# Kernel tuning notes

Hardware: AMD Instinct MI355X
Metric: run time of the kernel (lower is better)

The kernel has to match this reference:

```python
import jax, jax.numpy as jnp
import numpy as np

UNITS = 2048

def _cat_complex(Wr, Wi):
    # real-matrix representation of complex matmul: [[Wr, -Wi], [Wi, Wr]]
    top = jnp.concatenate([Wr, -Wi], axis=-1)
    bot = jnp.concatenate([Wi, Wr], axis=-1)
    return jnp.concatenate([top, bot], axis=0)

def _hard_sigmoid(x):
    return jnp.clip(0.2 * x + 0.5, 0.0, 1.0)

def setup_inputs() -> dict:
    key = jax.random.key(0)
    ks = jax.random.split(key, 8)
    B, IN2, U3 = 1024, 4096, 3 * UNITS
    s_in = 1.0 / np.sqrt(IN2)
    s_h = 1.0 / np.sqrt(2 * UNITS)
    return {
        "inputs": jax.random.normal(ks[0], (B, IN2), jnp.float32),
        "h_tm1": jax.random.normal(ks[1], (B, 2 * UNITS), jnp.float32),
        "real_kernel": jax.random.normal(ks[2], (IN2 // 2, U3), jnp.float32) * s_in,
        "imaginary_kernel": jax.random.normal(ks[3], (IN2 // 2, U3), jnp.float32) * s_in,
        "real_recurrent_kernel": jax.random.normal(ks[4], (UNITS, U3), jnp.float32) * s_h,
        "imaginary_recurrent_kernel": jax.random.normal(ks[5], (UNITS, U3), jnp.float32) * s_h,
        "real_bias": jax.random.normal(ks[6], (U3,), jnp.float32) * 0.01,
        "imaginary_bias": jax.random.normal(ks[7], (U3,), jnp.float32) * 0.01,
    }

def reference(inputs, h_tm1, real_kernel, imaginary_kernel,
              real_recurrent_kernel, imaginary_recurrent_kernel,
              real_bias, imaginary_bias):
    u = UNITS
    # per-gate complex kernels in real [[Wr,-Wi],[Wi,Wr]] form
    Kz = _cat_complex(real_kernel[:, :u], imaginary_kernel[:, :u])
    Kr = _cat_complex(real_kernel[:, u:2 * u], imaginary_kernel[:, u:2 * u])
    Kh = _cat_complex(real_kernel[:, 2 * u:], imaginary_kernel[:, 2 * u:])
    Rz = _cat_complex(real_recurrent_kernel[:, :u], imaginary_recurrent_kernel[:, :u])
    Rr = _cat_complex(real_recurrent_kernel[:, u:2 * u], imaginary_recurrent_kernel[:, u:2 * u])
    Rh = _cat_complex(real_recurrent_kernel[:, 2 * u:], imaginary_recurrent_kernel[:, 2 * u:])
    bz = jnp.concatenate([real_bias[:u], imaginary_bias[:u]])
    br = jnp.concatenate([real_bias[u:2 * u], imaginary_bias[u:2 * u]])
    bh = jnp.concatenate([real_bias[2 * u:], imaginary_bias[2 * u:]])
    # implementation=1, reset_after=False, no dropout
    x_z = inputs @ Kz + bz
    x_r = inputs @ Kr + br
    x_h = inputs @ Kh + bh
    z = _hard_sigmoid(x_z + h_tm1 @ Rz)
    r = _hard_sigmoid(x_r + h_tm1 @ Rr)
    hh = jnp.tanh(x_h + (r * h_tm1) @ Rh)
    h = z * h_tm1 + (1.0 - z) * hh
    return h
```

## Files before the change

### kernel.cpp

```cpp
#include <hip/hip_runtime.h>

typedef _Float16 half8  __attribute__((ext_vector_type(8)));
typedef _Float16 half4v __attribute__((ext_vector_type(4)));
typedef _Float16 half2v __attribute__((ext_vector_type(2)));
typedef float    float4v __attribute__((ext_vector_type(4)));

__device__ __forceinline__ float hsig(float x) {
  return fminf(fmaxf(fmaf(x, 0.2f, 0.5f), 0.0f), 1.0f);
}

__global__ __launch_bounds__(256) void cvt_pair(const float* __restrict__ src,
                                                _Float16* __restrict__ d1,
                                                _Float16* __restrict__ d2) {
  int i = blockIdx.x * blockDim.x + threadIdx.x;
  int base = i * 4;
  int j = base & 4095;
  float s = (j < 2048) ? -1.0f : 1.0f;
  float4 v = *(const float4*)&src[base];
  half4v h1 = {(_Float16)v.x, (_Float16)v.y, (_Float16)v.z, (_Float16)v.w};
  half4v h2 = {(_Float16)(s * v.x), (_Float16)(s * v.y), (_Float16)(s * v.z), (_Float16)(s * v.w)};
  *(half4v*)&d1[base] = h1;
  *(half4v*)&d2[base] = h2;
}

__global__ __launch_bounds__(256) void transpose_cast(
    const float* __restrict__ s0, const float* __restrict__ s1,
    const float* __restrict__ s2, const float* __restrict__ s3,
    _Float16* __restrict__ d0, _Float16* __restrict__ d1m,
    _Float16* __restrict__ d2m, _Float16* __restrict__ d3m)
{
  __shared__ float tile[64][65];
  const float* srcs[4] = {s0, s1, s2, s3};
  _Float16*    dsts[4] = {d0, d1m, d2m, d3m};
  const float* src = srcs[blockIdx.z];
  _Float16*    dst = dsts[blockIdx.z];

  const int tid = threadIdx.x;
  const int k0 = blockIdx.x * 64;
  const int j0 = blockIdx.y * 64;

  const int tx = tid & 63, ty = tid >> 6;
#pragma unroll
  for (int r = 0; r < 64; r += 4)
    tile[r + ty][tx] = src[(size_t)(k0 + r + ty) * 6144 + j0 + tx];
  __syncthreads();

  const int txk = (tid & 31) * 2;
  const int tyn = tid >> 5;
#pragma unroll
  for (int r = 0; r < 64; r += 8) {
    int jl = r + tyn;
    half2v p = {(_Float16)tile[txk][jl], (_Float16)tile[txk + 1][jl]};
    *(half2v*)&dst[(size_t)(j0 + jl) * 2048 + k0 + txk] = p;
  }
}

__global__ __launch_bounds__(256) void rgate(const _Float16* __restrict__ xacc,
                                             const float* __restrict__ h,
                                             _Float16* __restrict__ A1r,
                                             _Float16* __restrict__ A2r) {
  int i = blockIdx.x * blockDim.x + threadIdx.x;
  int base = i * 4;
  int m = base >> 12;
  int j = base & 4095;
  float s = (j < 2048) ? -1.0f : 1.0f;
  half4v rp = *(const half4v*)&xacc[(size_t)m * 12288 + 4096 + j];
  float4 hv = *(const float4*)&h[base];
  float p0 = hsig((float)rp[0]) * hv.x;
  float p1 = hsig((float)rp[1]) * hv.y;
  float p2 = hsig((float)rp[2]) * hv.z;
  float p3 = hsig((float)rp[3]) * hv.w;
  half4v o1 = {(_Float16)p0, (_Float16)p1, (_Float16)p2, (_Float16)p3};
  half4v o2 = {(_Float16)(s * p0), (_Float16)(s * p1), (_Float16)(s * p2), (_Float16)(s * p3)};
  *(half4v*)&A1r[base] = o1;
  *(half4v*)&A2r[base] = o2;
}

__global__ __launch_bounds__(256) void combine(const _Float16* __restrict__ xacc,
                                               const _Float16* __restrict__ P0,
                                               const _Float16* __restrict__ P1,
                                               const float* __restrict__ h,
                                               float* __restrict__ out) {
  int i = blockIdx.x * blockDim.x + threadIdx.x;
  int base = i * 4;
  int m = base >> 12;
  int j = base & 4095;
  half4v zv = *(const half4v*)&xacc[(size_t)m * 12288 + j];
  half4v xh = *(const half4v*)&xacc[(size_t)m * 12288 + 8192 + j];
  half4v p0 = *(const half4v*)&P0[base];
  half4v p1 = *(const half4v*)&P1[base];
  float4 hv = *(const float4*)&h[base];
  float4 o;
  {
    float z = hsig((float)zv[0]); float t = tanhf((float)xh[0] + (float)p0[0] + (float)p1[0]);
    o.x = z * hv.x + (1.0f - z) * t;
  }
  {
    float z = hsig((float)zv[1]); float t = tanhf((float)xh[1] + (float)p0[1] + (float)p1[1]);
    o.y = z * hv.y + (1.0f - z) * t;
  }
  {
    float z = hsig((float)zv[2]); float t = tanhf((float)xh[2] + (float)p0[2] + (float)p1[2]);
    o.z = z * hv.z + (1.0f - z) * t;
  }
  {
    float z = hsig((float)zv[3]); float t = tanhf((float)xh[3] + (float)p0[3] + (float)p1[3]);
    o.w = z * hv.w + (1.0f - z) * t;
  }
  *(float4*)&out[base] = o;
}

template<int FINAL>
__global__ __launch_bounds__(256, 3) void gemm_big(
    const _Float16* __restrict__ Ax1, const _Float16* __restrict__ Ax2,
    const _Float16* __restrict__ Ah1, const _Float16* __restrict__ Ah2,
    const _Float16* __restrict__ WKr, const _Float16* __restrict__ WKi,
    const _Float16* __restrict__ WRr, const _Float16* __restrict__ WRi,
    _Float16* __restrict__ xacc,
    _Float16* __restrict__ P0, _Float16* __restrict__ P1,
    const float* __restrict__ rbias, const float* __restrict__ ibias)
{
  __shared__ __align__(16) _Float16 lds[16384];
  const int tid  = threadIdx.x;
  const int lane = tid & 63;
  const int wave = tid >> 6;
  const int quad = lane >> 4;
  const int r16  = lane & 15;
  const int wm = (wave >> 1) * 64;
  const int wn = (wave & 1) * 64;
  const int mbase = blockIdx.y * 128;
  const int nbase = blockIdx.x * 128;

  const int  gate   = nbase >> 12;
  const bool hi     = (nbase & 2048) != 0;
  const int  jprime = nbase & 2047;

  int nph;
  const _Float16* pA[4];
  const _Float16* pB[4];
  if (FINAL) {
    nph = 1;
    const _Float16* Ax = hi ? Ax2 : Ax1;
    const _Float16* BL = hi ? WKi : WKr;
    const _Float16* BH = hi ? WKr : WKi;
    if (blockIdx.z == 0) {
      pA[0] = Ax + (size_t)mbase * 4096;
      pB[0] = BL + (size_t)jprime * 2048;
    } else {
      pA[0] = Ax + (size_t)mbase * 4096 + 2048;
      pB[0] = BH + (size_t)jprime * 2048;
    }
  } else {
    const size_t browK = (size_t)(gate * 2048 + jprime) * 2048;
    const _Float16* Ax = hi ? Ax2 : Ax1;
    const _Float16* KL = hi ? WKi : WKr;
    const _Float16* KH = hi ? WKr : WKi;
    pA[0] = Ax + (size_t)mbase * 4096;      pB[0] = KL + browK;
    pA[1] = pA[0] + 2048;                   pB[1] = KH + browK;
    if (gate < 2) {
      nph = 4;
      const _Float16* Ah = hi ? Ah2 : Ah1;
      const _Float16* RL = hi ? WRi : WRr;
      const _Float16* RH = hi ? WRr : WRi;
      pA[2] = Ah + (size_t)mbase * 4096;    pB[2] = RL + browK;
      pA[3] = pA[2] + 2048;                 pB[3] = RH + browK;
    } else {
      nph = 2;
    }
  }

  float4v acc[4][4];
#pragma unroll
  for (int i = 0; i < 4; ++i)
#pragma unroll
    for (int j = 0; j < 4; ++j) acc[i][j] = (float4v){0.f, 0.f, 0.f, 0.f};

  int offA[4], offB[4], ldsA[4], ldsB[4];
#pragma unroll
  for (int i = 0; i < 4; ++i) {
    int c = i * 256 + tid;
    int row = c >> 3;
    int sw = (c & 7) ^ (row & 7);
    offA[i] = row * 4096 + sw * 8;
    offB[i] = row * 2048 + sw * 8;
    ldsA[i] = c * 8;
    ldsB[i] = 8192 + c * 8;
  }

#pragma unroll 1
  for (int p = 0; p < 4; ++p) {
    if (p >= nph) break;
    const _Float16* Ab = pA[p];
    const _Float16* Bb = pB[p];
#pragma unroll 1
    for (int it = 0; it < 32; ++it) {
#pragma unroll
      for (int i = 0; i < 4; ++i)
        __builtin_amdgcn_global_load_lds(
            (__attribute__((address_space(1))) void*)(Ab + offA[i]),
            (__attribute__((address_space(3))) void*)&lds[ldsA[i]], 16, 0, 0);
#pragma unroll
      for (int i = 0; i < 4; ++i)
        __builtin_amdgcn_global_load_lds(
            (__attribute__((address_space(1))) void*)(Bb + offB[i]),
            (__attribute__((address_space(3))) void*)&lds[ldsB[i]], 16, 0, 0);
      Ab += 64;
      Bb += 64;
      __syncthreads();
#pragma unroll
      for (int ks = 0; ks < 2; ++ks) {
        half8 af[4], bf[4];
        int akg = ks * 4 + quad;
#pragma unroll
        for (int t = 0; t < 4; ++t) {
          int arow = wm + t * 16 + r16;
          af[t] = *(const half8*)&lds[(arow * 8 + (akg ^ (arow & 7))) * 8];
          int brow = wn + t * 16 + r16;
          bf[t] = *(const half8*)&lds[8192 + (brow * 8 + (akg ^ (brow & 7))) * 8];
        }
#pragma unroll
        for (int mt = 0; mt < 4; ++mt)
#pragma unroll
          for (int nt = 0; nt < 4; ++nt)
            acc[mt][nt] = __builtin_amdgcn_mfma_f32_16x16x32_f16(af[mt], bf[nt], acc[mt][nt], 0, 0, 0);
      }
      __syncthreads();
    }
  }

  const int mrow0 = mbase + wm + quad * 4;
  const int ncol0 = nbase + wn + r16;
  if (!FINAL) {
#pragma unroll
    for (int nt = 0; nt < 4; ++nt) {
      int n = ncol0 + nt * 16;
      int g = n >> 12, j = n & 4095;
      float b = (j < 2048) ? rbias[g * 2048 + j] : ibias[g * 2048 + j - 2048];
#pragma unroll
      for (int mt = 0; mt < 4; ++mt)
#pragma unroll
        for (int e = 0; e < 4; ++e) {
          int m = mrow0 + mt * 16 + e;
          xacc[(size_t)m * 12288 + n] = (_Float16)(acc[mt][nt][e] + b);
        }
    }
  } else {
    _Float16* P = blockIdx.z ? P1 : P0;
#pragma unroll
    for (int nt = 0; nt < 4; ++nt) {
      int n = ncol0 + nt * 16;
#pragma unroll
      for (int mt = 0; mt < 4; ++mt)
#pragma unroll
        for (int e = 0; e < 4; ++e) {
          int m = mrow0 + mt * 16 + e;
          P[(size_t)m * 4096 + n] = (_Float16)acc[mt][nt][e];
        }
    }
  }
}

extern "C" void kernel_launch(void* const* d_in, const int* in_sizes, int n_in,
                              void* d_out, int out_size, void* d_ws, size_t ws_size,
                              hipStream_t stream) {
  const float* inputs = (const float*)d_in[0];
  const float* h_tm1  = (const float*)d_in[1];
  const float* rk     = (const float*)d_in[2];
  const float* ik     = (const float*)d_in[3];
  const float* rrk    = (const float*)d_in[4];
  const float* irk    = (const float*)d_in[5];
  const float* rb     = (const float*)d_in[6];
  const float* ib     = (const float*)d_in[7];
  float* out = (float*)d_out;

  char* ws = (char*)d_ws;
  _Float16* WrK  = (_Float16*)(ws + 0);
  _Float16* WiK  = (_Float16*)(ws + 25165824);
  _Float16* WrR  = (_Float16*)(ws + 50331648);
  _Float16* WiR  = (_Float16*)(ws + 75497472);
  _Float16* A1x  = (_Float16*)(ws + 100663296);
  _Float16* A2x  = (_Float16*)(ws + 109051904);
  _Float16* A1h  = (_Float16*)(ws + 117440512);
  _Float16* A2h  = (_Float16*)(ws + 125829120);
  _Float16* xacc = (_Float16*)(ws + 134217728);
  _Float16* A1r  = A1x;
  _Float16* A2r  = A2x;
  _Float16* P0   = A1h;
  _Float16* P1   = A2h;

  cvt_pair<<<4096, 256, 0, stream>>>(inputs, A1x, A2x);
  cvt_pair<<<4096, 256, 0, stream>>>(h_tm1, A1h, A2h);
  transpose_cast<<<dim3(32, 96, 4), 256, 0, stream>>>(rk, ik, rrk, irk, WrK, WiK, WrR, WiR);
  gemm_big<0><<<dim3(96, 8), 256, 0, stream>>>(A1x, A2x, A1h, A2h, WrK, WiK, WrR, WiR,
                                               xacc, nullptr, nullptr, rb, ib);
  rgate<<<4096, 256, 0, stream>>>(xacc, h_tm1, A1r, A2r);
  gemm_big<1><<<dim3(32, 8, 2), 256, 0, stream>>>(A1r, A2r, nullptr, nullptr,
                                                  WrR + (size_t)4096 * 2048,
                                                  WiR + (size_t)4096 * 2048,
                                                  nullptr, nullptr, nullptr, P0, P1,
                                                  nullptr, nullptr);
  combine<<<4096, 256, 0, stream>>>(xacc, P0, P1, h_tm1, out);
}
```

Baseline: 504.5 us.

## Fuse final GRU combine into candidate GEMM epilogue and merge conversion launches

Replaces the split-K final GEMM (two fp16 partial outputs plus a separate combine kernel) with a single GEMM over both K halves using 64x128 tiles, whose epilogue applies the hard sigmoid, tanh and gated blend and writes the output directly. It also merges the two input conversion launches into one 2D launch and widens transpose_cast stores to 8 halves per thread. This removes the partial-sum round trip through global memory and two kernel launches. The trade-off is that the final GEMM now has a longer K loop per block with no split-K parallelism, and its epilogue does strided scalar loads from xacc and h_tm1.

```diff
diff --git a/kernel.cpp b/kernel.cpp
--- a/kernel.cpp
+++ b/kernel.cpp
@@ -9,9 +9,13 @@
   return fminf(fmaxf(fmaf(x, 0.2f, 0.5f), 0.0f), 1.0f);
 }
 
-__global__ __launch_bounds__(256) void cvt_pair(const float* __restrict__ src,
-                                                _Float16* __restrict__ d1,
-                                                _Float16* __restrict__ d2) {
+__global__ __launch_bounds__(256) void cvt_pair2(
+    const float* __restrict__ s0, const float* __restrict__ s1,
+    _Float16* __restrict__ d1a, _Float16* __restrict__ d2a,
+    _Float16* __restrict__ d1b, _Float16* __restrict__ d2b) {
+  const float* src = blockIdx.y ? s1 : s0;
+  _Float16* d1 = blockIdx.y ? d1b : d1a;
+  _Float16* d2 = blockIdx.y ? d2b : d2a;
   int i = blockIdx.x * blockDim.x + threadIdx.x;
   int base = i * 4;
   int j = base & 4095;
@@ -45,13 +49,15 @@
     tile[r + ty][tx] = src[(size_t)(k0 + r + ty) * 6144 + j0 + tx];
   __syncthreads();
 
-  const int txk = (tid & 31) * 2;
-  const int tyn = tid >> 5;
-#pragma unroll
-  for (int r = 0; r < 64; r += 8) {
-    int jl = r + tyn;
-    half2v p = {(_Float16)tile[txk][jl], (_Float16)tile[txk + 1][jl]};
-    *(half2v*)&dst[(size_t)(j0 + jl) * 2048 + k0 + txk] = p;
+  const int kc = tid & 7;
+  const int jr = tid >> 3;
+#pragma unroll
+  for (int r = 0; r < 64; r += 32) {
+    int jl = r + jr;
+    half8 p;
+#pragma unroll
+    for (int i = 0; i < 8; ++i) p[i] = (_Float16)tile[kc * 8 + i][jl];
+    *(half8*)&dst[(size_t)(j0 + jl) * 2048 + k0 + kc * 8] = p;
   }
 }
 
@@ -76,48 +82,12 @@
   *(half4v*)&A2r[base] = o2;
 }
 
-__global__ __launch_bounds__(256) void combine(const _Float16* __restrict__ xacc,
-                                               const _Float16* __restrict__ P0,
-                                               const _Float16* __restrict__ P1,
-                                               const float* __restrict__ h,
-                                               float* __restrict__ out) {
-  int i = blockIdx.x * blockDim.x + threadIdx.x;
-  int base = i * 4;
-  int m = base >> 12;
-  int j = base & 4095;
-  half4v zv = *(const half4v*)&xacc[(size_t)m * 12288 + j];
-  half4v xh = *(const half4v*)&xacc[(size_t)m * 12288 + 8192 + j];
-  half4v p0 = *(const half4v*)&P0[base];
-  half4v p1 = *(const half4v*)&P1[base];
-  float4 hv = *(const float4*)&h[base];
-  float4 o;
-  {
-    float z = hsig((float)zv[0]); float t = tanhf((float)xh[0] + (float)p0[0] + (float)p1[0]);
-    o.x = z * hv.x + (1.0f - z) * t;
-  }
-  {
-    float z = hsig((float)zv[1]); float t = tanhf((float)xh[1] + (float)p0[1] + (float)p1[1]);
-    o.y = z * hv.y + (1.0f - z) * t;
-  }
-  {
-    float z = hsig((float)zv[2]); float t = tanhf((float)xh[2] + (float)p0[2] + (float)p1[2]);
-    o.z = z * hv.z + (1.0f - z) * t;
-  }
-  {
-    float z = hsig((float)zv[3]); float t = tanhf((float)xh[3] + (float)p0[3] + (float)p1[3]);
-    o.w = z * hv.w + (1.0f - z) * t;
-  }
-  *(float4*)&out[base] = o;
-}
-
-template<int FINAL>
-__global__ __launch_bounds__(256, 3) void gemm_big(
+__global__ __launch_bounds__(256, 3) void gemm_fused(
     const _Float16* __restrict__ Ax1, const _Float16* __restrict__ Ax2,
     const _Float16* __restrict__ Ah1, const _Float16* __restrict__ Ah2,
     const _Float16* __restrict__ WKr, const _Float16* __restrict__ WKi,
     const _Float16* __restrict__ WRr, const _Float16* __restrict__ WRi,
     _Float16* __restrict__ xacc,
-    _Float16* __restrict__ P0, _Float16* __restrict__ P1,
     const float* __restrict__ rbias, const float* __restrict__ ibias)
 {
   __shared__ __align__(16) _Float16 lds[16384];
@@ -134,24 +104,12 @@
   const int  gate   = nbase >> 12;
   const bool hi     = (nbase & 2048) != 0;
   const int  jprime = nbase & 2047;
+  const size_t browK = (size_t)(gate * 2048 + jprime) * 2048;
 
   int nph;
   const _Float16* pA[4];
   const _Float16* pB[4];
-  if (FINAL) {
-    nph = 1;
-    const _Float16* Ax = hi ? Ax2 : Ax1;
-    const _Float16* BL = hi ? WKi : WKr;
-    const _Float16* BH = hi ? WKr : WKi;
-    if (blockIdx.z == 0) {
-      pA[0] = Ax + (size_t)mbase * 4096;
-      pB[0] = BL + (size_t)jprime * 2048;
-    } else {
-      pA[0] = Ax + (size_t)mbase * 4096 + 2048;
-      pB[0] = BH + (size_t)jprime * 2048;
-    }
-  } else {
-    const size_t browK = (size_t)(gate * 2048 + jprime) * 2048;
+  {
     const _Float16* Ax = hi ? Ax2 : Ax1;
     const _Float16* KL = hi ? WKi : WKr;
     const _Float16* KH = hi ? WKr : WKi;
@@ -230,33 +188,132 @@
 
   const int mrow0 = mbase + wm + quad * 4;
   const int ncol0 = nbase + wn + r16;
-  if (!FINAL) {
-#pragma unroll
-    for (int nt = 0; nt < 4; ++nt) {
-      int n = ncol0 + nt * 16;
-      int g = n >> 12, j = n & 4095;
-      float b = (j < 2048) ? rbias[g * 2048 + j] : ibias[g * 2048 + j - 2048];
-#pragma unroll
-      for (int mt = 0; mt < 4; ++mt)
-#pragma unroll
-        for (int e = 0; e < 4; ++e) {
-          int m = mrow0 + mt * 16 + e;
-          xacc[(size_t)m * 12288 + n] = (_Float16)(acc[mt][nt][e] + b);
+#pragma unroll
+  for (int nt = 0; nt < 4; ++nt) {
+    int n = ncol0 + nt * 16;
+    int g = n >> 12, j = n & 4095;
+    float b = (j < 2048) ? rbias[g * 2048 + j] : ibias[g * 2048 + j - 2048];
+#pragma unroll
+    for (int mt = 0; mt < 4; ++mt)
+#pragma unroll
+      for (int e = 0; e < 4; ++e) {
+        int m = mrow0 + mt * 16 + e;
+        xacc[(size_t)m * 12288 + n] = (_Float16)(acc[mt][nt][e] + b);
+      }
+  }
+}
+
+__global__ __launch_bounds__(256, 4) void gemm_final(
+    const _Float16* __restrict__ A1, const _Float16* __restrict__ A2,
+    const _Float16* __restrict__ Wr, const _Float16* __restrict__ Wi,
+    const _Float16* __restrict__ xacc, const float* __restrict__ h_tm1,
+    float* __restrict__ out)
+{
+  __shared__ __align__(16) _Float16 lds[12288];
+  const int tid  = threadIdx.x;
+  const int lane = tid & 63;
+  const int wave = tid >> 6;
+  const int quad = lane >> 4;
+  const int r16  = lane & 15;
+  const int wm = (wave >> 1) * 32;
+  const int wn = (wave & 1) * 64;
+  const int mbase = blockIdx.y * 64;
+  const int nbase = blockIdx.x * 128;
+
+  const bool hi     = (nbase & 2048) != 0;
+  const int  jprime = nbase & 2047;
+  const _Float16* A  = hi ? A2 : A1;
+  const _Float16* BL = hi ? Wi : Wr;
+  const _Float16* BH = hi ? Wr : Wi;
+
+  const _Float16* pA[2] = { A + (size_t)mbase * 4096,
+                            A + (size_t)mbase * 4096 + 2048 };
+  const _Float16* pB[2] = { BL + (size_t)jprime * 2048,
+                            BH + (size_t)jprime * 2048 };
+
+  float4v acc[2][4];
+#pragma unroll
+  for (int i = 0; i < 2; ++i)
+#pragma unroll
+    for (int j = 0; j < 4; ++j) acc[i][j] = (float4v){0.f, 0.f, 0.f, 0.f};
+
+  int offA[2], ldsA[2], offB[4], ldsB[4];
+#pragma unroll
+  for (int i = 0; i < 2; ++i) {
+    int c = i * 256 + tid;
+    int row = c >> 3;
+    int sw = (c & 7) ^ (row & 7);
+    offA[i] = row * 4096 + sw * 8;
+    ldsA[i] = c * 8;
+  }
+#pragma unroll
+  for (int i = 0; i < 4; ++i) {
+    int c = i * 256 + tid;
+    int row = c >> 3;
+    int sw = (c & 7) ^ (row & 7);
+    offB[i] = row * 2048 + sw * 8;
+    ldsB[i] = 4096 + c * 8;
+  }
+
+#pragma unroll 1
+  for (int p = 0; p < 2; ++p) {
+    const _Float16* Ab = pA[p];
+    const _Float16* Bb = pB[p];
+#pragma unroll 1
+    for (int it = 0; it < 32; ++it) {
+#pragma unroll
+      for (int i = 0; i < 2; ++i)
+        __builtin_amdgcn_global_load_lds(
+            (__attribute__((address_space(1))) void*)(Ab + offA[i]),
+            (__attribute__((address_space(3))) void*)&lds[ldsA[i]], 16, 0, 0);
+#pragma unroll
+      for (int i = 0; i < 4; ++i)
+        __builtin_amdgcn_global_load_lds(
+            (__attribute__((address_space(1))) void*)(Bb + offB[i]),
+            (__attribute__((address_space(3))) void*)&lds[ldsB[i]], 16, 0, 0);
+      Ab += 64;
+      Bb += 64;
+      __syncthreads();
+#pragma unroll
+      for (int ks = 0; ks < 2; ++ks) {
+        half8 af[2], bf[4];
+        int akg = ks * 4 + quad;
+#pragma unroll
+        for (int t = 0; t < 2; ++t) {
+          int arow = wm + t * 16 + r16;
+          af[t] = *(const half8*)&lds[(arow * 8 + (akg ^ (arow & 7))) * 8];
         }
+#pragma unroll
+        for (int t = 0; t < 4; ++t) {
+          int brow = wn + t * 16 + r16;
+          bf[t] = *(const half8*)&lds[4096 + (brow * 8 + (akg ^ (brow & 7))) * 8];
+        }
+#pragma unroll
+        for (int mt = 0; mt < 2; ++mt)
+#pragma unroll
+          for (int nt = 0; nt < 4; ++nt)
+            acc[mt][nt] = __builtin_amdgcn_mfma_f32_16x16x32_f16(af[mt], bf[nt], acc[mt][nt], 0, 0, 0);
+      }
+      __syncthreads();
     }
-  } else {
-    _Float16* P = blockIdx.z ? P1 : P0;
-#pragma unroll
-    for (int nt = 0; nt < 4; ++nt) {
-      int n = ncol0 + nt * 16;
-#pragma unroll
-      for (int mt = 0; mt < 4; ++mt)
-#pragma unroll
-        for (int e = 0; e < 4; ++e) {
-          int m = mrow0 + mt * 16 + e;
-          P[(size_t)m * 4096 + n] = (_Float16)acc[mt][nt][e];
-        }
-    }
+  }
+
+  const int mrow0 = mbase + wm + quad * 4;
+  const int ncol0 = nbase + wn + r16;
+#pragma unroll
+  for (int nt = 0; nt < 4; ++nt) {
+    int n = ncol0 + nt * 16;
+#pragma unroll
+    for (int mt = 0; mt < 2; ++mt)
+#pragma unroll
+      for (int e = 0; e < 4; ++e) {
+        int m = mrow0 + mt * 16 + e;
+        float z  = hsig((float)xacc[(size_t)m * 12288 + n]);
+        float xh = (float)xacc[(size_t)m * 12288 + 8192 + n];
+        float hh = tanhf(xh + acc[mt][nt][e]);
+        float ht = h_tm1[(size_t)m * 4096 + n];
+        out[(size_t)m * 4096 + n] = z * ht + (1.0f - z) * hh;
+      }
   }
 }
 
@@ -285,19 +342,14 @@
   _Float16* xacc = (_Float16*)(ws + 134217728);
   _Float16* A1r  = A1x;
   _Float16* A2r  = A2x;
-  _Float16* P0   = A1h;
-  _Float16* P1   = A2h;
-
-  cvt_pair<<<4096, 256, 0, stream>>>(inputs, A1x, A2x);
-  cvt_pair<<<4096, 256, 0, stream>>>(h_tm1, A1h, A2h);
+
+  cvt_pair2<<<dim3(4096, 2), 256, 0, stream>>>(inputs, h_tm1, A1x, A2x, A1h, A2h);
   transpose_cast<<<dim3(32, 96, 4), 256, 0, stream>>>(rk, ik, rrk, irk, WrK, WiK, WrR, WiR);
-  gemm_big<0><<<dim3(96, 8), 256, 0, stream>>>(A1x, A2x, A1h, A2h, WrK, WiK, WrR, WiR,
-                                               xacc, nullptr, nullptr, rb, ib);
+  gemm_fused<<<dim3(96, 8), 256, 0, stream>>>(A1x, A2x, A1h, A2h, WrK, WiK, WrR, WiR,
+                                              xacc, rb, ib);
   rgate<<<4096, 256, 0, stream>>>(xacc, h_tm1, A1r, A2r);
-  gemm_big<1><<<dim3(32, 8, 2), 256, 0, stream>>>(A1r, A2r, nullptr, nullptr,
-                                                  WrR + (size_t)4096 * 2048,
-                                                  WiR + (size_t)4096 * 2048,
-                                                  nullptr, nullptr, nullptr, P0, P1,
-                                                  nullptr, nullptr);
-  combine<<<4096, 256, 0, stream>>>(xacc, P0, P1, h_tm1, out);
-}
+  gemm_final<<<dim3(32, 16), 256, 0, stream>>>(A1r, A2r,
+                                               WrR + (size_t)4096 * 2048,
+                                               WiR + (size_t)4096 * 2048,
+                                               xacc, h_tm1, out);
+}
```

New measurement: 508.1 us. Within noise of the previous version (+0.7%).
